# Kernel tuning notes

Measured on AMD Instinct MI355X. Metric: run time of the kernel, lower is better.

Reference implementation:

```python
import jax, jax.numpy as jnp
import numpy as np

# Static module configuration (matches init_kwargs; img_spacing defaults to 1)
SIZE = (160, 192, 160)
SPACING = (8.0, 8.0, 8.0)
CP = tuple(int((s - 1) // sp + 4) for s, sp in zip(SIZE, SPACING))  # (23, 27, 23)


def _axis_weights_pivots(n, sp):
    """Per-axis cubic B-spline weights [n,4] and control-point indices [n,4]."""
    v = jnp.arange(n, dtype=jnp.float32) / sp
    f = jnp.floor(v)
    d = v - f  # fractional part in [0,1)
    w = jnp.stack([
        (1.0 - d) ** 3 / 6.0,                               # idx == 0
        d ** 3 / 2.0 - d ** 2 + 2.0 / 3.0,                  # idx == 1
        -d ** 3 / 2.0 + d ** 2 / 2.0 + d / 2.0 + 1.0 / 6.0, # idx == 2
        d ** 3 / 6.0,                                       # idx == 3
    ], axis=-1)  # [n, 4]
    p = f.astype(jnp.int32)[:, None] + jnp.arange(4, dtype=jnp.int32)[None, :]  # [n, 4]
    return w, p


def setup_inputs() -> dict:
    key = jax.random.key(0)
    mesh = jax.random.normal(key, (4, 3, *CP), dtype=jnp.float32)
    return {"mesh": mesh}


def reference(mesh):
    # Separable tensor-product form of the 4^3-offset gather-MAC loop:
    # flow[b,c,x,y,z] = sum_{a,b2,c2} wX[x,a]*wY[y,b2]*wZ[z,c2]
    #                    * mesh[b,c, fX[x]+a, fY[y]+b2, fZ[z]+c2]
    wx, px = _axis_weights_pivots(SIZE[0], SPACING[0])
    wy, py = _axis_weights_pivots(SIZE[1], SPACING[1])
    wz, pz = _axis_weights_pivots(SIZE[2], SPACING[2])
    # gather+contract along x: [B,C,X,4,CY,CZ] x [X,4] -> [B,C,X,CY,CZ]
    t = jnp.einsum('bcxakl,xa->bcxkl', mesh[:, :, px, :, :], wx)
    # gather+contract along y: [B,C,X,Y,4,CZ] x [Y,4] -> [B,C,X,Y,CZ]
    t = jnp.einsum('bcxyal,ya->bcxyl', t[:, :, :, py, :], wy)
    # gather+contract along z: [B,C,X,Y,Z,4] x [Z,4] -> [B,C,X,Y,Z]
    flow = jnp.einsum('bcxyza,za->bcxyz', t[:, :, :, :, pz], wz)
    return flow
```

## Files before the change

### kernel.cpp

```cpp
#include <hip/hip_runtime.h>


#define SPX 160
#define SPY 192
#define SPZ 160
#define CPX 23
#define CPY 27
#define CPZ 23
#define CZP 25

__global__ __launch_bounds__(256, 8) void ffd_kernel(const float* __restrict__ mesh,
                                                     float* __restrict__ out) {
    const int yb  = blockIdx.x;
    const int xb  = blockIdx.y;
    const int bc  = blockIdx.z;
    const int tid = threadIdx.x;

    __shared__ __align__(16) float wlds[8][4];
    __shared__ float tX[8][4][CZP];
    __shared__ float tXY[8][8][CZP];

    if (tid < 32) {
        int j = tid >> 2, a = tid & 3;
        float d  = (float)j * 0.125f;
        float d2 = d * d, d3 = d2 * d;
        float w;
        if (a == 0)      { float e = 1.0f - d; w = e * e * e * (1.0f / 6.0f); }
        else if (a == 1) { w = 0.5f * d3 - d2 + (2.0f / 3.0f); }
        else if (a == 2) { w = -0.5f * d3 + 0.5f * d2 + 0.5f * d + (1.0f / 6.0f); }
        else             { w = d3 * (1.0f / 6.0f); }
        wlds[j][a] = w;
    }
    __syncthreads();

    const float* mch = mesh + (size_t)bc * (CPX * CPY * CPZ);
    for (int i = tid; i < 8 * 4 * CPZ; i += 256) {
        int cz = i % CPZ;
        int r  = i / CPZ;
        int b2 = r & 3;
        int x8 = r >> 2;
        const float* mp = mch + (size_t)xb * (CPY * CPZ) + (yb + b2) * CPZ + cz;
        float acc = wlds[x8][0] * mp[0]
                  + wlds[x8][1] * mp[CPY * CPZ]
                  + wlds[x8][2] * mp[2 * CPY * CPZ]
                  + wlds[x8][3] * mp[3 * CPY * CPZ];
        tX[x8][b2][cz] = acc;
    }
    __syncthreads();

    for (int i = tid; i < 8 * 8 * CPZ; i += 256) {
        int cz = i % CPZ;
        int r  = i / CPZ;
        int y8 = r & 7;
        int x8 = r >> 3;
        float acc = wlds[y8][0] * tX[x8][0][cz]
                  + wlds[y8][1] * tX[x8][1][cz]
                  + wlds[y8][2] * tX[x8][2][cz]
                  + wlds[y8][3] * tX[x8][3][cz];
        tXY[x8][y8][cz] = acc;
    }
    __syncthreads();

    const int zt = tid & 7;
    const int h  = zt & 1;
    const int qo = zt >> 1;

    const float4 Wr0 = *(const float4*)&wlds[4 * h + 0][0];
    const float4 Wr1 = *(const float4*)&wlds[4 * h + 1][0];
    const float4 Wr2 = *(const float4*)&wlds[4 * h + 2][0];
    const float4 Wr3 = *(const float4*)&wlds[4 * h + 3][0];

    float* oblk = out + ((size_t)bc * SPX * SPY
                       + (size_t)(xb * 8) * SPY
                       + (size_t)(yb * 8)) * SPZ;
    #pragma unroll
    for (int pass = 0; pass < 2; ++pass) {
        int row = pass * 32 + (tid >> 3);
        int x8 = row >> 3, y8 = row & 7;
        const float* trow = &tXY[x8][y8][0];
        float* orow = oblk + ((size_t)x8 * SPY + (size_t)y8) * SPZ;
        #pragma unroll
        for (int k = 0; k < 5; ++k) {
            int qa = 4 * k + qo;
            float m0 = trow[qa];
            float m1 = trow[qa + 1];
            float m2 = trow[qa + 2];
            float m3 = trow[qa + 3];
            float4 o;
            o.x = Wr0.x * m0 + Wr0.y * m1 + Wr0.z * m2 + Wr0.w * m3;
            o.y = Wr1.x * m0 + Wr1.y * m1 + Wr1.z * m2 + Wr1.w * m3;
            o.z = Wr2.x * m0 + Wr2.y * m1 + Wr2.z * m2 + Wr2.w * m3;
            o.w = Wr3.x * m0 + Wr3.y * m1 + Wr3.z * m2 + Wr3.w * m3;
            *(float4*)&orow[32 * k + 4 * zt] = o;
        }
    }
}

extern "C" void kernel_launch(void* const* d_in, const int* in_sizes, int n_in,
                              void* d_out, int out_size, void* d_ws, size_t ws_size,
                              hipStream_t stream) {
    const float* mesh = (const float*)d_in[0];
    float* out = (float*)d_out;
    dim3 grid(SPY / 8, SPX / 8, 4 * 3);
    ffd_kernel<<<grid, 256, 0, stream>>>(mesh, out);
}
```

Baseline: 42.59 us.

## Process three y-tiles per block with double-buffered LDS pipeline

Each block now handles three consecutive y tiles instead of one, shrinking the grid from 24 to 8 blocks along y. The x-contraction for the next tile is computed while the current tile's output is being written, and the xy intermediate is double-buffered in LDS. A lighter barrier macro waits only on LDS counters before s_barrier, so the global stores are not drained at each sync. This amortizes weight setup and launch overhead and overlaps mesh loads with stores, at the cost of fewer blocks (less parallelism) and more LDS per block.

```diff
diff --git a/kernel.cpp b/kernel.cpp
--- a/kernel.cpp
+++ b/kernel.cpp
@@ -9,16 +9,19 @@
 #define CPZ 23
 #define CZP 25
 
+#define BAR() do { asm volatile("s_waitcnt lgkmcnt(0)" ::: "memory"); \
+                   __builtin_amdgcn_s_barrier(); } while (0)
+
 __global__ __launch_bounds__(256, 8) void ffd_kernel(const float* __restrict__ mesh,
                                                      float* __restrict__ out) {
-    const int yb  = blockIdx.x;
+    const int ybg = blockIdx.x;
     const int xb  = blockIdx.y;
     const int bc  = blockIdx.z;
     const int tid = threadIdx.x;
 
     __shared__ __align__(16) float wlds[8][4];
     __shared__ float tX[8][4][CZP];
-    __shared__ float tXY[8][8][CZP];
+    __shared__ float tXY[2][8][8][CZP];
 
     if (tid < 32) {
         int j = tid >> 2, a = tid & 3;
@@ -34,65 +37,87 @@
     __syncthreads();
 
     const float* mch = mesh + (size_t)bc * (CPX * CPY * CPZ);
-    for (int i = tid; i < 8 * 4 * CPZ; i += 256) {
-        int cz = i % CPZ;
-        int r  = i / CPZ;
-        int b2 = r & 3;
-        int x8 = r >> 2;
-        const float* mp = mch + (size_t)xb * (CPY * CPZ) + (yb + b2) * CPZ + cz;
-        float acc = wlds[x8][0] * mp[0]
-                  + wlds[x8][1] * mp[CPY * CPZ]
-                  + wlds[x8][2] * mp[2 * CPY * CPZ]
-                  + wlds[x8][3] * mp[3 * CPY * CPZ];
-        tX[x8][b2][cz] = acc;
-    }
-    __syncthreads();
 
-    for (int i = tid; i < 8 * 8 * CPZ; i += 256) {
-        int cz = i % CPZ;
-        int r  = i / CPZ;
-        int y8 = r & 7;
-        int x8 = r >> 3;
-        float acc = wlds[y8][0] * tX[x8][0][cz]
-                  + wlds[y8][1] * tX[x8][1][cz]
-                  + wlds[y8][2] * tX[x8][2][cz]
-                  + wlds[y8][3] * tX[x8][3][cz];
-        tXY[x8][y8][cz] = acc;
-    }
-    __syncthreads();
+    auto stageA = [&](int yb) {
+        for (int i = tid; i < 8 * 4 * CPZ; i += 256) {
+            int cz = i % CPZ;
+            int r  = i / CPZ;
+            int b2 = r & 3;
+            int x8 = r >> 2;
+            const float* mp = mch + (size_t)xb * (CPY * CPZ) + (yb + b2) * CPZ + cz;
+            float acc = wlds[x8][0] * mp[0]
+                      + wlds[x8][1] * mp[CPY * CPZ]
+                      + wlds[x8][2] * mp[2 * CPY * CPZ]
+                      + wlds[x8][3] * mp[3 * CPY * CPZ];
+            tX[x8][b2][cz] = acc;
+        }
+    };
+
+    auto stageB = [&](int buf) {
+        for (int i = tid; i < 8 * 8 * CPZ; i += 256) {
+            int cz = i % CPZ;
+            int r  = i / CPZ;
+            int y8 = r & 7;
+            int x8 = r >> 3;
+            float acc = wlds[y8][0] * tX[x8][0][cz]
+                      + wlds[y8][1] * tX[x8][1][cz]
+                      + wlds[y8][2] * tX[x8][2][cz]
+                      + wlds[y8][3] * tX[x8][3][cz];
+            tXY[buf][x8][y8][cz] = acc;
+        }
+    };
 
     const int zt = tid & 7;
     const int h  = zt & 1;
     const int qo = zt >> 1;
-
     const float4 Wr0 = *(const float4*)&wlds[4 * h + 0][0];
     const float4 Wr1 = *(const float4*)&wlds[4 * h + 1][0];
     const float4 Wr2 = *(const float4*)&wlds[4 * h + 2][0];
     const float4 Wr3 = *(const float4*)&wlds[4 * h + 3][0];
 
-    float* oblk = out + ((size_t)bc * SPX * SPY
-                       + (size_t)(xb * 8) * SPY
-                       + (size_t)(yb * 8)) * SPZ;
+    auto stageC = [&](int yb, int buf) {
+        float* oblk = out + ((size_t)bc * SPX * SPY
+                           + (size_t)(xb * 8) * SPY
+                           + (size_t)(yb * 8)) * SPZ;
+        #pragma unroll
+        for (int pass = 0; pass < 2; ++pass) {
+            int row = pass * 32 + (tid >> 3);
+            int x8 = row >> 3, y8 = row & 7;
+            const float* trow = &tXY[buf][x8][y8][0];
+            float* orow = oblk + ((size_t)x8 * SPY + (size_t)y8) * SPZ;
+            #pragma unroll
+            for (int k = 0; k < 5; ++k) {
+                int qa = 4 * k + qo;
+                float m0 = trow[qa];
+                float m1 = trow[qa + 1];
+                float m2 = trow[qa + 2];
+                float m3 = trow[qa + 3];
+                float4 o;
+                o.x = Wr0.x * m0 + Wr0.y * m1 + Wr0.z * m2 + Wr0.w * m3;
+                o.y = Wr1.x * m0 + Wr1.y * m1 + Wr1.z * m2 + Wr1.w * m3;
+                o.z = Wr2.x * m0 + Wr2.y * m1 + Wr2.z * m2 + Wr2.w * m3;
+                o.w = Wr3.x * m0 + Wr3.y * m1 + Wr3.z * m2 + Wr3.w * m3;
+                *(float4*)&orow[32 * k + 4 * zt] = o;
+            }
+        }
+    };
+
+    const int yb0 = ybg * 3;
+
+    stageA(yb0);
+    BAR();
+    stageB(0);
+    BAR();
+
+    int cur = 0;
     #pragma unroll
-    for (int pass = 0; pass < 2; ++pass) {
-        int row = pass * 32 + (tid >> 3);
-        int x8 = row >> 3, y8 = row & 7;
-        const float* trow = &tXY[x8][y8][0];
-        float* orow = oblk + ((size_t)x8 * SPY + (size_t)y8) * SPZ;
-        #pragma unroll
-        for (int k = 0; k < 5; ++k) {
-            int qa = 4 * k + qo;
-            float m0 = trow[qa];
-            float m1 = trow[qa + 1];
-            float m2 = trow[qa + 2];
-            float m3 = trow[qa + 3];
-            float4 o;
-            o.x = Wr0.x * m0 + Wr0.y * m1 + Wr0.z * m2 + Wr0.w * m3;
-            o.y = Wr1.x * m0 + Wr1.y * m1 + Wr1.z * m2 + Wr1.w * m3;
-            o.z = Wr2.x * m0 + Wr2.y * m1 + Wr2.z * m2 + Wr2.w * m3;
-            o.w = Wr3.x * m0 + Wr3.y * m1 + Wr3.z * m2 + Wr3.w * m3;
-            *(float4*)&orow[32 * k + 4 * zt] = o;
-        }
+    for (int t = 0; t < 3; ++t) {
+        if (t < 2) stageA(yb0 + t + 1);
+        stageC(yb0 + t, cur);
+        BAR();
+        if (t < 2) stageB(cur ^ 1);
+        BAR();
+        cur ^= 1;
     }
 }
 
@@ -101,6 +126,6 @@
                               hipStream_t stream) {
     const float* mesh = (const float*)d_in[0];
     float* out = (float*)d_out;
-    dim3 grid(SPY / 8, SPX / 8, 4 * 3);
+    dim3 grid(8, SPX / 8, 4 * 3);
     ffd_kernel<<<grid, 256, 0, stream>>>(mesh, out);
 }
```

New measurement: 43.60 us. 2.4% more time.

## Transpose LDS intermediates to cz-major layout, unroll stages, add nontemporal stores

Applied to the files above, without the earlier changes.

The shared-memory intermediates tX and tXY become cz-major with padded strides (32 and 72). Stage two can then read four tX values with one float4 LDS load, and the index math loses its integer division and modulo by 23. The first two stage loops are fully unrolled with a guard on the tail iteration. Output stores become nontemporal vector stores to reduce cache pollution from the large write stream. In exchange, the global mesh reads in stage one now follow a different thread-to-address mapping, and the final-stage LDS reads are strided, which may cause bank conflicts.

```diff
diff --git a/kernel.cpp b/kernel.cpp
--- a/kernel.cpp
+++ b/kernel.cpp
@@ -7,7 +7,11 @@
 #define CPX 23
 #define CPY 27
 #define CPZ 23
-#define CZP 25
+
+#define TXS  32
+#define TXYS 72
+
+typedef float vfloat4 __attribute__((ext_vector_type(4)));
 
 __global__ __launch_bounds__(256, 8) void ffd_kernel(const float* __restrict__ mesh,
                                                      float* __restrict__ out) {
@@ -17,8 +21,8 @@
     const int tid = threadIdx.x;
 
     __shared__ __align__(16) float wlds[8][4];
-    __shared__ float tX[8][4][CZP];
-    __shared__ float tXY[8][8][CZP];
+    __shared__ __align__(16) float tX[CPZ * TXS];
+    __shared__ __align__(16) float tXY[CPZ * TXYS];
 
     if (tid < 32) {
         int j = tid >> 2, a = tid & 3;
@@ -33,38 +37,39 @@
     }
     __syncthreads();
 
-    const float* mch = mesh + (size_t)bc * (CPX * CPY * CPZ);
-    for (int i = tid; i < 8 * 4 * CPZ; i += 256) {
-        int cz = i % CPZ;
-        int r  = i / CPZ;
-        int b2 = r & 3;
-        int x8 = r >> 2;
-        const float* mp = mch + (size_t)xb * (CPY * CPZ) + (yb + b2) * CPZ + cz;
-        float acc = wlds[x8][0] * mp[0]
-                  + wlds[x8][1] * mp[CPY * CPZ]
-                  + wlds[x8][2] * mp[2 * CPY * CPZ]
-                  + wlds[x8][3] * mp[3 * CPY * CPZ];
-        tX[x8][b2][cz] = acc;
+    const float* mbase = mesh + (size_t)bc * (CPX * CPY * CPZ)
+                              + (size_t)xb * (CPY * CPZ) + (size_t)yb * CPZ;
+    #pragma unroll
+    for (int j = 0; j < 3; ++j) {
+        int i = tid + 256 * j;
+        if (j < 2 || tid < 736 - 512) {
+            int b2 = i & 3, x8 = (i >> 2) & 7, cz = i >> 5;
+            const float* mp = mbase + b2 * CPZ + cz;
+            float acc = wlds[x8][0] * mp[0]
+                      + wlds[x8][1] * mp[CPY * CPZ]
+                      + wlds[x8][2] * mp[2 * CPY * CPZ]
+                      + wlds[x8][3] * mp[3 * CPY * CPZ];
+            tX[cz * TXS + x8 * 4 + b2] = acc;
+        }
     }
     __syncthreads();
 
-    for (int i = tid; i < 8 * 8 * CPZ; i += 256) {
-        int cz = i % CPZ;
-        int r  = i / CPZ;
-        int y8 = r & 7;
-        int x8 = r >> 3;
-        float acc = wlds[y8][0] * tX[x8][0][cz]
-                  + wlds[y8][1] * tX[x8][1][cz]
-                  + wlds[y8][2] * tX[x8][2][cz]
-                  + wlds[y8][3] * tX[x8][3][cz];
-        tXY[x8][y8][cz] = acc;
+    #pragma unroll
+    for (int j = 0; j < 6; ++j) {
+        int i = tid + 256 * j;
+        if (j < 5 || tid < 1472 - 1280) {
+            int y8 = i & 7, x8 = (i >> 3) & 7, cz = i >> 6;
+            const float4 t4 = *(const float4*)&tX[cz * TXS + x8 * 4];
+            float acc = wlds[y8][0] * t4.x + wlds[y8][1] * t4.y
+                      + wlds[y8][2] * t4.z + wlds[y8][3] * t4.w;
+            tXY[cz * TXYS + x8 * 8 + y8] = acc;
+        }
     }
     __syncthreads();
 
     const int zt = tid & 7;
     const int h  = zt & 1;
     const int qo = zt >> 1;
-
     const float4 Wr0 = *(const float4*)&wlds[4 * h + 0][0];
     const float4 Wr1 = *(const float4*)&wlds[4 * h + 1][0];
     const float4 Wr2 = *(const float4*)&wlds[4 * h + 2][0];
@@ -77,21 +82,21 @@
     for (int pass = 0; pass < 2; ++pass) {
         int row = pass * 32 + (tid >> 3);
         int x8 = row >> 3, y8 = row & 7;
-        const float* trow = &tXY[x8][y8][0];
+        const float* tcol = &tXY[x8 * 8 + y8];
         float* orow = oblk + ((size_t)x8 * SPY + (size_t)y8) * SPZ;
         #pragma unroll
         for (int k = 0; k < 5; ++k) {
             int qa = 4 * k + qo;
-            float m0 = trow[qa];
-            float m1 = trow[qa + 1];
-            float m2 = trow[qa + 2];
-            float m3 = trow[qa + 3];
-            float4 o;
+            float m0 = tcol[qa * TXYS];
+            float m1 = tcol[(qa + 1) * TXYS];
+            float m2 = tcol[(qa + 2) * TXYS];
+            float m3 = tcol[(qa + 3) * TXYS];
+            vfloat4 o;
             o.x = Wr0.x * m0 + Wr0.y * m1 + Wr0.z * m2 + Wr0.w * m3;
             o.y = Wr1.x * m0 + Wr1.y * m1 + Wr1.z * m2 + Wr1.w * m3;
             o.z = Wr2.x * m0 + Wr2.y * m1 + Wr2.z * m2 + Wr2.w * m3;
             o.w = Wr3.x * m0 + Wr3.y * m1 + Wr3.z * m2 + Wr3.w * m3;
-            *(float4*)&orow[32 * k + 4 * zt] = o;
+            __builtin_nontemporal_store(o, (vfloat4*)&orow[32 * k + 4 * zt]);
         }
     }
 }
```

Result: slower. 49.03 us (+15.1%).
